# Kernel tuning notes

Hardware: AMD Instinct MI355X
Metric: run time of the kernel (lower is better)

Reference implementation:

```python
import jax, jax.numpy as jnp
import numpy as np

D_H = 128
N_RBF = 16
R_MIN = 0.0
R_MAX = float(np.sqrt(2.0))


def _rbf(r):
    # Gaussian RBF expansion: centers linspace(R_MIN, R_MAX, N_RBF),
    # width = center spacing, exp(-(r-mu)^2 / (2*width^2))
    centers = jnp.linspace(R_MIN, R_MAX, N_RBF, dtype=r.dtype)
    width = (R_MAX - R_MIN) / (N_RBF - 1)
    gamma = 1.0 / (2.0 * width * width)
    return jnp.exp(-gamma * (r[:, None] - centers[None, :]) ** 2)


def setup_inputs() -> dict:
    key = jax.random.key(0)
    ks = jax.random.split(key, 16)
    N, E = 50000, 800000
    h = jax.random.normal(ks[0], (N, D_H), dtype=jnp.float32)
    x = jax.random.uniform(ks[1], (N, 2), dtype=jnp.float32)
    edge_index = jax.random.randint(ks[2], (2, E), 0, N, dtype=jnp.int64)
    edge_weight = jax.random.uniform(ks[3], (E,), dtype=jnp.float32)

    def lin(k, fan_in, fan_out):
        s = 1.0 / np.sqrt(fan_in)
        kw, kb = jax.random.split(k)
        W = jax.random.uniform(kw, (fan_in, fan_out), minval=-s, maxval=s, dtype=jnp.float32)
        b = jax.random.uniform(kb, (fan_out,), minval=-s, maxval=s, dtype=jnp.float32)
        return W, b

    Wm1, bm1 = lin(ks[4], 2 * D_H + N_RBF, D_H)
    Wm2, bm2 = lin(ks[5], D_H, D_H)
    Wh1, bh1 = lin(ks[6], 2 * D_H, D_H)
    Wh2, bh2 = lin(ks[7], D_H, D_H)
    ln_g = jnp.ones((D_H,), dtype=jnp.float32)
    ln_b = jnp.zeros((D_H,), dtype=jnp.float32)
    return {"h": h, "x": x, "edge_index": edge_index, "edge_weight": edge_weight,
            "Wm1": Wm1, "bm1": bm1, "Wm2": Wm2, "bm2": bm2,
            "Wh1": Wh1, "bh1": bh1, "Wh2": Wh2, "bh2": bh2,
            "ln_g": ln_g, "ln_b": ln_b}


def reference(h, x, edge_index, edge_weight, Wm1, bm1, Wm2, bm2, Wh1, bh1, Wh2, bh2, ln_g, ln_b):
    N = h.shape[0]
    src = edge_index[0]
    dst = edge_index[1]
    # per-edge geometry
    dx = x[src, :2] - x[dst, :2]                      # [E,2]
    r = jnp.sqrt(jnp.sum(dx * dx, axis=-1) + 1e-8)    # [E]
    rbf = _rbf(r)                                     # [E,n_rbf]
    # message MLP: Linear -> SiLU -> Linear
    m_in = jnp.concatenate([h[src], h[dst], rbf], axis=-1)  # [E, 2*d_h+n_rbf]
    m = jax.nn.silu(m_in @ Wm1 + bm1) @ Wm2 + bm2            # [E, d_h]
    m = m * edge_weight[:, None]
    # scatter-sum aggregate into destination nodes
    agg = jax.ops.segment_sum(m, dst, num_segments=N)        # [N, d_h]
    # node update MLP
    u_in = jnp.concatenate([h, agg], axis=-1)                # [N, 2*d_h]
    h_up = jax.nn.silu(u_in @ Wh1 + bh1) @ Wh2 + bh2         # [N, d_h]
    # residual + LayerNorm
    z = h + h_up
    mu = jnp.mean(z, axis=-1, keepdims=True)
    var = jnp.var(z, axis=-1, keepdims=True)
    return (z - mu) / jnp.sqrt(var + 1e-5) * ln_g + ln_b
```

## Files before the change

kernel.cpp:

```cpp
#include <hip/hip_runtime.h>
#include <hip/hip_bf16.h>
#include <math.h>

#define DH 128
#define NRBF 16
#define EB 128
#define NTAB 1025
#define SEGCAP 32

typedef unsigned short ushort_t;
typedef __attribute__((ext_vector_type(8))) short short8;
typedef __attribute__((ext_vector_type(4))) float floatx4;

__device__ __forceinline__ float silu_f(float v) {
    return v / (1.f + __expf(-v));
}
__device__ __forceinline__ unsigned pk_bf16(float lo, float hi) {
    __hip_bfloat162 h = __float22bfloat162_rn(make_float2(lo, hi));
    union { __hip_bfloat162 h2; unsigned u; } cv;
    cv.h2 = h;
    return cv.u;
}
__device__ __forceinline__ ushort_t f2bf1(float f) {
    unsigned u = __float_as_uint(f);
    u += 0x7FFFu + ((u >> 16) & 1u);
    return (ushort_t)(u >> 16);
}
__device__ __forceinline__ float bflo(unsigned u) { return __uint_as_float(u << 16); }
__device__ __forceinline__ float bfhi(unsigned u) { return __uint_as_float(u & 0xffff0000u); }
__device__ __forceinline__ float bf2f(ushort_t u) { return __uint_as_float(((unsigned)u) << 16); }

__device__ __forceinline__ int detect64(const int* __restrict__ ei) {
    int z = 0;
#pragma unroll
    for (int i = 0; i < 8; ++i) z |= ei[2 * i + 1];
    return (z == 0) ? 1 : 0;
}
__device__ __forceinline__ int load_dst(const int* ei, int is64, int e, int E) {
    return is64 ? ei[2 * E + 2 * e] : ei[E + e];
}
__device__ __forceinline__ int load_src(const int* ei, int is64, int e, int E) {
    return is64 ? ei[2 * e] : ei[e];
}

__global__ __launch_bounds__(256) void k_hist_prep(
    const int* __restrict__ ei, int* __restrict__ counts, int E,
    const float* __restrict__ Wm1, const float* __restrict__ Wm2,
    const float* __restrict__ Wh1, const float* __restrict__ Wh2,
    ushort_t* __restrict__ Tbf, ushort_t* __restrict__ W2f,
    ushort_t* __restrict__ W1mf, ushort_t* __restrict__ W1hf,
    ushort_t* __restrict__ W2hf, int nb_hist)
{
    const int b = blockIdx.x, tid = threadIdx.x;
    if (b < nb_hist) {
        const int e = b * 256 + tid;
        if (e < E) {
            const int is64 = detect64(ei);
            atomicAdd(&counts[load_dst(ei, is64, e, E)], 1);
        }
        return;
    }
    int b2 = b - nb_hist;
    if (b2 < 257) {
        const int i = b2 * 4 + (tid >> 6);
        if (i < NTAB) {
            const float WIDTH = 0.09428090415820634f;
            const float GAMMA = 56.25f;
            const float DELTA = 1.4142135623730951f / 1024.0f;
            const float r = (float)i * DELTA;
            const int c0 = (tid & 63) * 2;
            float a0 = 0.f, a1 = 0.f;
#pragma unroll
            for (int q = 0; q < NRBF; ++q) {
                const float dr = r - (float)q * WIDTH;
                const float w = __expf(-GAMMA * dr * dr);
                a0 = fmaf(w, Wm1[(256 + q) * DH + c0], a0);
                a1 = fmaf(w, Wm1[(256 + q) * DH + c0 + 1], a1);
            }
            *(unsigned*)(Tbf + (size_t)i * DH + c0) = pk_bf16(a0, a1);
        }
        return;
    }
    b2 -= 257;
    if (b2 < 8) {
        const int u = b2 * 256 + tid;
        const int col = u & 127, kclg = u >> 7;
        const int lg = kclg & 3, kc = kclg >> 2;
        unsigned o[4];
#pragma unroll
        for (int j = 0; j < 2; ++j) {
            o[j]     = pk_bf16(Wm2[(kc * 32 + 4 * lg + 2 * j) * DH + col],
                               Wm2[(kc * 32 + 4 * lg + 2 * j + 1) * DH + col]);
            o[2 + j] = pk_bf16(Wm2[(kc * 32 + 16 + 4 * lg + 2 * j) * DH + col],
                               Wm2[(kc * 32 + 16 + 4 * lg + 2 * j + 1) * DH + col]);
        }
        *(uint4*)(W2f + 8 * u) = make_uint4(o[0], o[1], o[2], o[3]);
        return;
    }
    b2 -= 8;
    if (b2 < 16) {
        const int u = b2 * 256 + tid;
        const int c = u & 255, kclg = u >> 8;
        const int lg = kclg & 3, kc = kclg >> 2;
        const int base = (c < 128) ? 0 : 128;
        const int cc = c & 127;
        unsigned o[4];
#pragma unroll
        for (int j = 0; j < 2; ++j) {
            o[j]     = pk_bf16(Wm1[(base + kc * 32 + 4 * lg + 2 * j) * DH + cc],
                               Wm1[(base + kc * 32 + 4 * lg + 2 * j + 1) * DH + cc]);
            o[2 + j] = pk_bf16(Wm1[(base + kc * 32 + 16 + 4 * lg + 2 * j) * DH + cc],
                               Wm1[(base + kc * 32 + 16 + 4 * lg + 2 * j + 1) * DH + cc]);
        }
        *(uint4*)(W1mf + 8 * u) = make_uint4(o[0], o[1], o[2], o[3]);
        return;
    }
    b2 -= 16;
    if (b2 < 16) {
        const int u = b2 * 256 + tid;
        const int col = u & 127, kclg = u >> 7;
        const int lg = kclg & 3, kc = kclg >> 2;
        unsigned o[4];
#pragma unroll
        for (int j = 0; j < 2; ++j) {
            o[j]     = pk_bf16(Wh1[(kc * 32 + 4 * lg + 2 * j) * DH + col],
                               Wh1[(kc * 32 + 4 * lg + 2 * j + 1) * DH + col]);
            o[2 + j] = pk_bf16(Wh1[(kc * 32 + 16 + 4 * lg + 2 * j) * DH + col],
                               Wh1[(kc * 32 + 16 + 4 * lg + 2 * j + 1) * DH + col]);
        }
        *(uint4*)(W1hf + 8 * u) = make_uint4(o[0], o[1], o[2], o[3]);
        return;
    }
    b2 -= 16;
    {
        const int u = b2 * 256 + tid;
        const int col = u & 127, kclg = u >> 7;
        const int lg = kclg & 3, kc = kclg >> 2;
        unsigned o[4];
#pragma unroll
        for (int j = 0; j < 2; ++j) {
            o[j]     = pk_bf16(Wh2[(kc * 32 + 4 * lg + 2 * j) * DH + col],
                               Wh2[(kc * 32 + 4 * lg + 2 * j + 1) * DH + col]);
            o[2 + j] = pk_bf16(Wh2[(kc * 32 + 16 + 4 * lg + 2 * j) * DH + col],
                               Wh2[(kc * 32 + 16 + 4 * lg + 2 * j + 1) * DH + col]);
        }
        *(uint4*)(W2hf + 8 * u) = make_uint4(o[0], o[1], o[2], o[3]);
    }
}

__global__ __launch_bounds__(1024) void k_scan(const int* __restrict__ counts,
                                               int* __restrict__ cursor, int N) {
    __shared__ int wsum[16];
    __shared__ int sCarry;
    const int tid = threadIdx.x, lane = tid & 63, wid = tid >> 6;
    if (tid == 0) sCarry = 0;
    __syncthreads();
    for (int c0 = 0; c0 < N; c0 += 4096) {
        const int idx = c0 + tid * 4;
        int4 v = make_int4(0, 0, 0, 0);
        if (idx < N) v = *(const int4*)(counts + idx);
        const int t01 = v.x + v.y;
        const int t012 = t01 + v.z;
        const int tot = t012 + v.w;
        int incl = tot;
#pragma unroll
        for (int d = 1; d < 64; d <<= 1) {
            int t = __shfl_up(incl, d, 64);
            if (lane >= d) incl += t;
        }
        if (lane == 63) wsum[wid] = incl;
        __syncthreads();
        if (wid == 0) {
            int s = (lane < 16) ? wsum[lane] : 0;
#pragma unroll
            for (int d = 1; d < 16; d <<= 1) {
                int t = __shfl_up(s, d, 64);
                if (lane >= d) s += t;
            }
            if (lane < 16) wsum[lane] = s;
        }
        __syncthreads();
        const int ex = sCarry + (wid > 0 ? wsum[wid - 1] : 0) + incl - tot;
        if (idx + 3 < N) {
            *(int4*)(cursor + idx) = make_int4(ex, ex + v.x, ex + t01, ex + t012);
        } else if (idx < N) {
            cursor[idx] = ex;
            if (idx + 1 < N) cursor[idx + 1] = ex + v.x;
            if (idx + 2 < N) cursor[idx + 2] = ex + t01;
        }
        __syncthreads();
        if (tid == 0) sCarry += wsum[15];
        __syncthreads();
    }
}

__global__ __launch_bounds__(256) void k_scatter_pre(
    const int* __restrict__ ei, const float* __restrict__ ew, const float* __restrict__ x,
    int* __restrict__ cursor, uint2* __restrict__ spk, int* __restrict__ dstS,
    int E, int pack,
    const float* __restrict__ h, const float* __restrict__ bm1,
    const ushort_t* __restrict__ W1mf,
    ushort_t* __restrict__ Abf, ushort_t* __restrict__ Bbf, int N, int nb_scat)
{
    const int tid = threadIdx.x;

    if ((int)blockIdx.x < nb_scat) {
        const int e = blockIdx.x * 256 + tid;
        if (e < E) {
            const int is64 = detect64(ei);
            const int s = load_src(ei, is64, e, E);
            const int d = load_dst(ei, is64, e, E);
            const int pos = atomicAdd(&cursor[d], 1);
            unsigned x0 = (unsigned)s;
            if (pack) {
                const float2 xs = *(const float2*)(x + 2 * s);
                const float2 xd = *(const float2*)(x + 2 * d);
                const float dxv = xs.x - xd.x, dyv = xs.y - xd.y;
                const float r = sqrtf(dxv * dxv + dyv * dyv + 1e-8f);
                int ti = (int)(r * 724.0773439350246f + 0.5f);
                ti = min(ti, NTAB - 1);
                x0 |= ((unsigned)ti << 16);
            }
            spk[pos] = make_uint2(x0, __float_as_uint(ew[e]));
            dstS[pos] = d;
        }
        return;
    }

    __shared__ __align__(16) ushort_t sIn[64 * DH];
    const int nblk = ((int)blockIdx.x - nb_scat) * 64;

    {
        const int row = tid >> 2, q = tid & 3;
        const int gn = nblk + row;
        const float4* ps = (const float4*)(h + (size_t)gn * DH + 32 * q);
        uint4* rowp = (uint4*)(sIn + row * DH);
        const int swz = row & 7;
#pragma unroll
        for (int i = 0; i < 4; ++i) {
            uint4 o = make_uint4(0, 0, 0, 0);
            if (gn < N) {
                const float4 g0 = ps[2 * i], g1 = ps[2 * i + 1];
                o.x = pk_bf16(g0.x, g0.y); o.y = pk_bf16(g0.z, g0.w);
                o.z = pk_bf16(g1.x, g1.y); o.w = pk_bf16(g1.z, g1.w);
            }
            rowp[(4 * q + i) ^ swz] = o;
        }
    }
    __syncthreads();

    const int lane = tid & 63, wv = tid >> 6;
    const int lr = lane & 15, lg = lane >> 4;
    const int m0l = wv * 16;

    union FragU { unsigned u[4]; short8 s8; };
    floatx4 acc[16];
#pragma unroll
    for (int ni = 0; ni < 16; ++ni) acc[ni] = (floatx4){0.f, 0.f, 0.f, 0.f};

#pragma unroll
    for (int kc = 0; kc < 4; ++kc) {
        const int b1 = 64 * kc + 8 * lg;
        const int b2 = b1 + 32;
        const int row = m0l + lr;
        const char* rbase = (const char*)(sIn + row * DH);
        const int swz = (row & 7) << 4;
        FragU af;
        const uint2 lo = *(const uint2*)(rbase + ((b1 & ~15) ^ swz) + (b1 & 15));
        const uint2 hi = *(const uint2*)(rbase + ((b2 & ~15) ^ swz) + (b2 & 15));
        af.u[0] = lo.x; af.u[1] = lo.y; af.u[2] = hi.x; af.u[3] = hi.y;
        const ushort_t* wbase = W1mf + ((size_t)(kc * 4 + lg) * 256 + lr) * 8;
        __builtin_amdgcn_s_setprio(1);
#pragma unroll
        for (int ni = 0; ni < 16; ++ni) {
            const short8 bf = *(const short8*)(wbase + ni * 128);
            acc[ni] = __builtin_amdgcn_mfma_f32_16x16x32_bf16(af.s8, bf, acc[ni], 0, 0, 0);
        }
        __builtin_amdgcn_s_setprio(0);
    }

    float bm1v[8];
#pragma unroll
    for (int ni = 0; ni < 8; ++ni) bm1v[ni] = bm1[ni * 16 + lr];
#pragma unroll
    for (int r = 0; r < 4; ++r) {
        const int gn = nblk + m0l + 4 * lg + r;
        if (gn < N) {
#pragma unroll
            for (int ni = 0; ni < 8; ++ni)
                Abf[(size_t)gn * DH + ni * 16 + lr] = f2bf1(acc[ni][r] + bm1v[ni]);
#pragma unroll
            for (int ni = 8; ni < 16; ++ni)
                Bbf[(size_t)gn * DH + (ni - 8) * 16 + lr] = f2bf1(acc[ni][r]);
        }
    }
}

__global__ __launch_bounds__(256, 4) void k_edge(
    const float* __restrict__ x, const int* __restrict__ ei, const float* __restrict__ ew,
    const uint2* __restrict__ spk, const int* __restrict__ dstS,
    const ushort_t* __restrict__ W2f, const float* __restrict__ bm2,
    const ushort_t* __restrict__ Abf, const ushort_t* __restrict__ Bbf,
    const ushort_t* __restrict__ Tbf, float* __restrict__ agg,
    int sorted, int pack, int N, int E)
{
    __shared__ __align__(16) ushort_t sHid[64 * DH];
    __shared__ __align__(16) float ldsAgg[SEGCAP][DH];
    __shared__ int   sSrc[EB];
    __shared__ int   sDst[EB];
    __shared__ int   sLid[EB];
    __shared__ int   sTi[EB];
    __shared__ float sEw[EB];
    __shared__ int   sSegStart[SEGCAP];
    __shared__ int   sNseg, sW0tot;

    const int tid = threadIdx.x;

    const int nwg = gridDim.x;
    const int xcd = blockIdx.x & 7;
    const int cidx = blockIdx.x >> 3;
    const int qch = nwg >> 3, rch = nwg & 7;
    const int bid = (xcd < rch) ? (xcd * (qch + 1) + cidx)
                                : (rch * (qch + 1) + (xcd - rch) * qch + cidx);
    const int e0 = bid * EB;

    {
        const float4 z = make_float4(0.f, 0.f, 0.f, 0.f);
        float4* za = (float4*)&ldsAgg[0][0];
#pragma unroll
        for (int i = 0; i < 4; ++i) za[tid + 256 * i] = z;
    }

    if (tid < EB) {
        const int slot = e0 + tid;
        int s = 0, d = 0, ti = 0;
        float w = 0.f;
        if (slot < E) {
            if (sorted) {
                const uint2 v = spk[slot];
                d = dstS[slot];
                w = __uint_as_float(v.y);
                if (pack) { s = (int)(v.x & 0xFFFFu); ti = (int)(v.x >> 16); }
                else {
                    s = (int)v.x;
                    const float2 xs = *(const float2*)(x + 2 * s);
                    const float2 xd = *(const float2*)(x + 2 * d);
                    const float dxv = xs.x - xd.x, dyv = xs.y - xd.y;
                    const float r = sqrtf(dxv * dxv + dyv * dyv + 1e-8f);
                    ti = min((int)(r * 724.0773439350246f + 0.5f), NTAB - 1);
                }
            } else {
                const int is64 = detect64(ei);
                s = load_src(ei, is64, slot, E);
                d = load_dst(ei, is64, slot, E);
                w = ew[slot];
                const float2 xs = *(const float2*)(x + 2 * s);
                const float2 xd = *(const float2*)(x + 2 * d);
                const float dxv = xs.x - xd.x, dyv = xs.y - xd.y;
                const float r = sqrtf(dxv * dxv + dyv * dyv + 1e-8f);
                ti = min((int)(r * 724.0773439350246f + 0.5f), NTAB - 1);
            }
        } else {
            d = sorted ? dstS[E - 1] : load_dst(ei, detect64(ei), E - 1, E);
        }
        sSrc[tid] = s; sDst[tid] = d; sEw[tid] = w; sTi[tid] = ti;
    }
    __syncthreads();

    int bflag = 0, incl = 0;
    if (tid < EB) {
        bflag = (tid > 0) && (sDst[tid] != sDst[tid - 1]);
        incl = bflag;
#pragma unroll
        for (int dd = 1; dd < 64; dd <<= 1) {
            int t = __shfl_up(incl, dd, 64);
            if ((tid & 63) >= dd) incl += t;
        }
    }
    if (tid == 63) sW0tot = incl;
    __syncthreads();
    if (tid >= 64 && tid < EB) incl += sW0tot;
    if (tid < EB) {
        sLid[tid] = incl;
        if ((bflag || tid == 0) && incl < SEGCAP) sSegStart[incl] = tid;
        if (tid == EB - 1) sNseg = incl + 1;
    }
    __syncthreads();

    const int lane = tid & 63;
    const int wv   = tid >> 6;
    const int lr   = lane & 15;
    const int lg   = lane >> 4;
    const int m0l  = (wv & 1) * 32;
    const int n0   = (wv >> 1) * 64;

    float bc4[4];
#pragma unroll
    for (int ni = 0; ni < 4; ++ni) bc4[ni] = bm2[n0 + ni * 16 + lr];

    union FragU { unsigned u[4]; short8 s8; };

    for (int half = 0; half < 2; ++half) {
        const int eh = half * 64;

        {
            const int el = tid >> 2;
            const int q  = tid & 3;
            const int le = eh + el;
            const int s  = sSrc[le];
            const int ti = sTi[le];
            const uint4* pA = (const uint4*)(Abf + (size_t)s * DH + 32 * q);
            const uint4* pB = (const uint4*)(Bbf + (size_t)sDst[le] * DH + 32 * q);
            const uint4* pT = (const uint4*)(Tbf + (size_t)ti * DH + 32 * q);
            uint4* rowp = (uint4*)(sHid + el * DH);
            const int swz = el & 7;
#pragma unroll
            for (int i = 0; i < 4; ++i) {
                const uint4 a = pA[i];
                const uint4 b = pB[i];
                const uint4 t = pT[i];
                const float v0 = bflo(a.x) + bflo(b.x) + bflo(t.x);
                const float v1 = bfhi(a.x) + bfhi(b.x) + bfhi(t.x);
                const float v2 = bflo(a.y) + bflo(b.y) + bflo(t.y);
                const float v3 = bfhi(a.y) + bfhi(b.y) + bfhi(t.y);
                const float v4 = bflo(a.z) + bflo(b.z) + bflo(t.z);
                const float v5 = bfhi(a.z) + bfhi(b.z) + bfhi(t.z);
                const float v6 = bflo(a.w) + bflo(b.w) + bflo(t.w);
                const float v7 = bfhi(a.w) + bfhi(b.w) + bfhi(t.w);
                uint4 pk;
                pk.x = pk_bf16(silu_f(v0), silu_f(v1));
                pk.y = pk_bf16(silu_f(v2), silu_f(v3));
                pk.z = pk_bf16(silu_f(v4), silu_f(v5));
                pk.w = pk_bf16(silu_f(v6), silu_f(v7));
                rowp[(4 * q + i) ^ swz] = pk;
            }
        }
        __syncthreads();

        floatx4 acc[2][4];
#pragma unroll
        for (int mi = 0; mi < 2; ++mi)
#pragma unroll
            for (int ni = 0; ni < 4; ++ni) acc[mi][ni] = (floatx4){0.f, 0.f, 0.f, 0.f};

#pragma unroll
        for (int kc = 0; kc < 4; ++kc) {
            const int b1 = 64 * kc + 8 * lg;
            const int b2 = b1 + 32;
            FragU af[2];
#pragma unroll
            for (int mi = 0; mi < 2; ++mi) {
                const int le2 = m0l + mi * 16 + lr;
                const char* rbase = (const char*)(sHid + le2 * DH);
                const int swz = (le2 & 7) << 4;
                const uint2 lo = *(const uint2*)(rbase + ((b1 & ~15) ^ swz) + (b1 & 15));
                const uint2 hi = *(const uint2*)(rbase + ((b2 & ~15) ^ swz) + (b2 & 15));
                af[mi].u[0] = lo.x; af[mi].u[1] = lo.y;
                af[mi].u[2] = hi.x; af[mi].u[3] = hi.y;
            }
            const ushort_t* wbase = W2f + ((size_t)(kc * 4 + lg) * 128 + n0 + lr) * 8;
            __builtin_amdgcn_s_setprio(1);
#pragma unroll
            for (int ni = 0; ni < 4; ++ni) {
                const short8 bf = *(const short8*)(wbase + ni * 128);
                acc[0][ni] = __builtin_amdgcn_mfma_f32_16x16x32_bf16(af[0].s8, bf, acc[0][ni], 0, 0, 0);
                acc[1][ni] = __builtin_amdgcn_mfma_f32_16x16x32_bf16(af[1].s8, bf, acc[1][ni], 0, 0, 0);
            }
            __builtin_amdgcn_s_setprio(0);
        }

        int   lid4[2][4];
        float ew4[2][4];
        int   hs[2];
#pragma unroll
        for (int mi = 0; mi < 2; ++mi) {
            const int sb = eh + m0l + mi * 16 + 4 * lg;
            hs[mi] = sb;
#pragma unroll
            for (int r = 0; r < 4; ++r) { lid4[mi][r] = sLid[sb + r]; ew4[mi][r] = sEw[sb + r]; }
        }
#pragma unroll
        for (int ni = 0; ni < 4; ++ni) {
            const int col = n0 + ni * 16 + lr;
            const float bc = bc4[ni];
#pragma unroll
            for (int mi = 0; mi < 2; ++mi) {
                int cur = lid4[mi][0], curSlot = hs[mi];
                float av = (acc[mi][ni][0] + bc) * ew4[mi][0];
#pragma unroll
                for (int r = 1; r < 4; ++r) {
                    const int l2 = lid4[mi][r];
                    const float v = (acc[mi][ni][r] + bc) * ew4[mi][r];
                    if (l2 == cur) av += v;
                    else {
                        if (cur < SEGCAP) atomicAdd(&ldsAgg[cur][col], av);
                        else atomicAdd(agg + (size_t)sDst[curSlot] * DH + col, av);
                        cur = l2; curSlot = hs[mi] + r; av = v;
                    }
                }
                if (cur < SEGCAP) atomicAdd(&ldsAgg[cur][col], av);
                else atomicAdd(agg + (size_t)sDst[curSlot] * DH + col, av);
            }
        }
        __syncthreads();
    }

    const int ns = sNseg;
    const int gmax = (ns < SEGCAP) ? ns : SEGCAP;
    for (int idx = tid; idx < (gmax << 7); idx += 256) {
        const int g = idx >> 7, col = idx & 127;
        const float v = ldsAgg[g][col];
        const int dst = sDst[sSegStart[g]];
        float* p = agg + (size_t)dst * DH + col;
        if (sorted && g > 0 && g < ns - 1) *p = v;
        else atomicAdd(p, v);
    }
}

__global__ __launch_bounds__(256) void k_node(
    const float* __restrict__ h, const float* __restrict__ agg,
    const ushort_t* __restrict__ W1hf, const float* __restrict__ bh1,
    const ushort_t* __restrict__ W2hf, const float* __restrict__ bh2,
    const float* __restrict__ ln_g, const float* __restrict__ ln_b,
    float* __restrict__ out, int N)
{
    __shared__ __align__(16) ushort_t sIn[64 * 256];
    __shared__ __align__(16) ushort_t sHid[64 * DH];
    const int tid = threadIdx.x;
    const int nblk = blockIdx.x * 64;

    {
        const int row = tid >> 2, q = tid & 3;
        const int gn = nblk + row;
        const float4* ps = (q < 2) ? (const float4*)(h + (size_t)gn * DH + 64 * q)
                                   : (const float4*)(agg + (size_t)gn * DH + 64 * (q - 2));
        uint4* rowp = (uint4*)(sIn + row * 256);
        const int swz = row & 7;
#pragma unroll
        for (int i = 0; i < 8; ++i) {
            uint4 o = make_uint4(0, 0, 0, 0);
            if (gn < N) {
                const float4 g0 = ps[2 * i], g1 = ps[2 * i + 1];
                o.x = pk_bf16(g0.x, g0.y); o.y = pk_bf16(g0.z, g0.w);
                o.z = pk_bf16(g1.x, g1.y); o.w = pk_bf16(g1.z, g1.w);
            }
            rowp[(8 * q + i) ^ swz] = o;
        }
    }
    __syncthreads();

    const int lane = tid & 63, wv = tid >> 6;
    const int lr = lane & 15, lg = lane >> 4;
    const int m0l = wv * 16;

    union FragU { unsigned u[4]; short8 s8; };

    floatx4 acc[8];
#pragma unroll
    for (int ni = 0; ni < 8; ++ni) acc[ni] = (floatx4){0.f, 0.f, 0.f, 0.f};

#pragma unroll
    for (int kc = 0; kc < 8; ++kc) {
        const int b1 = 64 * kc + 8 * lg;
        const int b2 = b1 + 32;
        const int row = m0l + lr;
        const char* rbase = (const char*)(sIn + row * 256);
        const int swz = (row & 7) << 4;
        FragU af;
        const uint2 lo = *(const uint2*)(rbase + ((b1 & ~15) ^ swz) + (b1 & 15));
        const uint2 hi = *(const uint2*)(rbase + ((b2 & ~15) ^ swz) + (b2 & 15));
        af.u[0] = lo.x; af.u[1] = lo.y; af.u[2] = hi.x; af.u[3] = hi.y;
        const ushort_t* wbase = W1hf + ((size_t)(kc * 4 + lg) * 128 + lr) * 8;
        __builtin_amdgcn_s_setprio(1);
#pragma unroll
        for (int ni = 0; ni < 8; ++ni) {
            const short8 bf = *(const short8*)(wbase + ni * 128);
            acc[ni] = __builtin_amdgcn_mfma_f32_16x16x32_bf16(af.s8, bf, acc[ni], 0, 0, 0);
        }
        __builtin_amdgcn_s_setprio(0);
    }

    {
        float bh1v[8];
#pragma unroll
        for (int ni = 0; ni < 8; ++ni) bh1v[ni] = bh1[ni * 16 + lr];
#pragma unroll
        for (int r = 0; r < 4; ++r) {
            const int row = m0l + 4 * lg + r;
            const int swz = row & 7;
            ushort_t* rp = sHid + row * DH;
#pragma unroll
            for (int ni = 0; ni < 8; ++ni) {
                const int col = ni * 16 + lr;
                rp[(((col >> 3) ^ swz) << 3) + (col & 7)] =
                    f2bf1(silu_f(acc[ni][r] + bh1v[ni]));
            }
        }
    }

    floatx4 acc2[8];
#pragma unroll
    for (int ni = 0; ni < 8; ++ni) acc2[ni] = (floatx4){0.f, 0.f, 0.f, 0.f};

#pragma unroll
    for (int kc = 0; kc < 4; ++kc) {
        const int b1 = 64 * kc + 8 * lg;
        const int b2 = b1 + 32;
        const int row = m0l + lr;
        const char* rbase = (const char*)(sHid + row * DH);
        const int swz = (row & 7) << 4;
        FragU af;
        const uint2 lo = *(const uint2*)(rbase + ((b1 & ~15) ^ swz) + (b1 & 15));
        const uint2 hi = *(const uint2*)(rbase + ((b2 & ~15) ^ swz) + (b2 & 15));
        af.u[0] = lo.x; af.u[1] = lo.y; af.u[2] = hi.x; af.u[3] = hi.y;
        const ushort_t* wbase = W2hf + ((size_t)(kc * 4 + lg) * 128 + lr) * 8;
        __builtin_amdgcn_s_setprio(1);
#pragma unroll
        for (int ni = 0; ni < 8; ++ni) {
            const short8 bf = *(const short8*)(wbase + ni * 128);
            acc2[ni] = __builtin_amdgcn_mfma_f32_16x16x32_bf16(af.s8, bf, acc2[ni], 0, 0, 0);
        }
        __builtin_amdgcn_s_setprio(0);
    }

    float gv[8], bv[8], b2v[8];
#pragma unroll
    for (int ni = 0; ni < 8; ++ni) {
        const int col = ni * 16 + lr;
        gv[ni] = ln_g[col]; bv[ni] = ln_b[col]; b2v[ni] = bh2[col];
    }
#pragma unroll
    for (int r = 0; r < 4; ++r) {
        const int row = m0l + 4 * lg + r;
        const int gn = nblk + row;
        const int swz = row & 7;
        float z[8];
        float s1 = 0.f, s2 = 0.f;
#pragma unroll
        for (int ni = 0; ni < 8; ++ni) {
            const int col = ni * 16 + lr;
            const float hv = bf2f(sIn[row * 256 + (((col >> 3) ^ swz) << 3) + (col & 7)]);
            z[ni] = acc2[ni][r] + b2v[ni] + hv;
            s1 += z[ni]; s2 += z[ni] * z[ni];
        }
#pragma unroll
        for (int m = 1; m < 16; m <<= 1) {
            s1 += __shfl_xor(s1, m, 64);
            s2 += __shfl_xor(s2, m, 64);
        }
        const float mean = s1 * (1.f / 128.f);
        const float var = s2 * (1.f / 128.f) - mean * mean;
        const float rstd = rsqrtf(var + 1e-5f);
        if (gn < N) {
#pragma unroll
            for (int ni = 0; ni < 8; ++ni) {
                const int col = ni * 16 + lr;
                out[(size_t)gn * DH + col] = (z[ni] - mean) * rstd * gv[ni] + bv[ni];
            }
        }
    }
}

extern "C" void kernel_launch(void* const* d_in, const int* in_sizes, int n_in,
                              void* d_out, int out_size, void* d_ws, size_t ws_size,
                              hipStream_t stream)
{
    (void)n_in; (void)out_size;
    const float* h   = (const float*)d_in[0];
    const float* x   = (const float*)d_in[1];
    const int*   ei  = (const int*)d_in[2];
    const float* ew  = (const float*)d_in[3];
    const float* Wm1 = (const float*)d_in[4];
    const float* bm1 = (const float*)d_in[5];
    const float* Wm2 = (const float*)d_in[6];
    const float* bm2 = (const float*)d_in[7];
    const float* Wh1 = (const float*)d_in[8];
    const float* bh1 = (const float*)d_in[9];
    const float* Wh2 = (const float*)d_in[10];
    const float* bh2 = (const float*)d_in[11];
    const float* lng = (const float*)d_in[12];
    const float* lnb = (const float*)d_in[13];
    float* out = (float*)d_out;

    const int N = in_sizes[0] / DH;
    const int E = in_sizes[3];

    float*    agg  = (float*)d_ws;
    ushort_t* Abf  = (ushort_t*)(agg + (size_t)N * DH);
    ushort_t* Bbf  = Abf + (size_t)N * DH;
    ushort_t* W2f  = Bbf + (size_t)N * DH;
    ushort_t* Tbf  = W2f + 16384;
    ushort_t* W1mf = Tbf + (size_t)NTAB * DH;
    ushort_t* W1hf = W1mf + 32768;
    ushort_t* W2hf = W1hf + 32768;
    int*   counts  = (int*)(W2hf + 16384);
    int*   cursor  = counts + N;
    uint2* spk     = (uint2*)(cursor + N);
    int*   dstS    = (int*)(spk + E);

    const size_t mand = (size_t)N * DH * 4 + (size_t)N * DH * 4
                      + ((size_t)16384 + (size_t)NTAB * DH + 32768 + 32768 + 16384) * 2;
    const size_t need = mand + (size_t)(2 * N) * 4 + (size_t)E * 12 + 64;
    const int use_sort = (ws_size >= need) ? 1 : 0;
    const int pack = use_sort && (N <= 65535);

    const int nb_hist = use_sort ? (E + 255) / 256 : 0;
    const int nb_prep = 257 + 8 + 16 + 16 + 8;
    const int nb_scat = nb_hist;
    const int nb_pre  = (N + 63) / 64;

    hipMemsetAsync(agg, 0, (size_t)N * DH * sizeof(float), stream);
    if (use_sort)
        hipMemsetAsync(counts, 0, (size_t)N * sizeof(int), stream);
    k_hist_prep<<<nb_hist + nb_prep, 256, 0, stream>>>(ei, counts, E, Wm1, Wm2, Wh1, Wh2,
                                                       Tbf, W2f, W1mf, W1hf, W2hf, nb_hist);
    if (use_sort)
        k_scan<<<1, 1024, 0, stream>>>(counts, cursor, N);
    k_scatter_pre<<<nb_scat + nb_pre, 256, 0, stream>>>(ei, ew, x, cursor, spk, dstS, E, pack,
                                                        h, bm1, W1mf, Abf, Bbf, N, nb_scat);
    k_edge<<<(E + EB - 1) / EB, 256, 0, stream>>>(x, ei, ew, spk, dstS,
                                                  W2f, bm2, Abf, Bbf, Tbf, agg,
                                                  use_sort, pack, N, E);
    k_node<<<(N + 63) / 64, 256, 0, stream>>>(h, agg, W1hf, bh1, W2hf, bh2, lng, lnb, out, N);
}
```

Baseline: 436.8 us.

## Restructure edge kernel into per-wave 16-edge tiles with early prefetched gathers

```diff
diff --git a/kernel.cpp b/kernel.cpp
--- a/kernel.cpp
+++ b/kernel.cpp
@@ -304,7 +304,7 @@
     const ushort_t* __restrict__ Tbf, float* __restrict__ agg,
     int sorted, int pack, int N, int E)
 {
-    __shared__ __align__(16) ushort_t sHid[64 * DH];
+    __shared__ __align__(16) ushort_t sHid[4][16 * DH];
     __shared__ __align__(16) float ldsAgg[SEGCAP][DH];
     __shared__ int   sSrc[EB];
     __shared__ int   sDst[EB];
@@ -314,7 +314,14 @@
     __shared__ int   sSegStart[SEGCAP];
     __shared__ int   sNseg, sW0tot;
 
-    const int tid = threadIdx.x;
+    const int tid  = threadIdx.x;
+    const int lane = tid & 63;
+    const int wv   = tid >> 6;
+    const int lr   = lane & 15;
+    const int lg   = lane >> 4;
+    const int e4   = lane >> 2;
+    const int q    = lane & 3;
+    const int wbase = wv * 32;
 
     const int nwg = gridDim.x;
     const int xcd = blockIdx.x & 7;
@@ -323,6 +330,29 @@
     const int bid = (xcd < rch) ? (xcd * (qch + 1) + cidx)
                                 : (rch * (qch + 1) + (xcd - rch) * qch + cidx);
     const int e0 = bid * EB;
+
+    const int fast = sorted && pack;
+
+    uint4 a0[4], b0[4], t0v[4], a1[4], b1[4], t1v[4];
+    int d1g = 0, t1g = 0;
+    if (fast) {
+        const int sl0 = min(e0 + wbase + e4, E - 1);
+        const int sl1 = min(e0 + wbase + 16 + e4, E - 1);
+        const uint2 v0 = spk[sl0], v1 = spk[sl1];
+        const int s0g = (int)(v0.x & 0xFFFFu), t0g = (int)(v0.x >> 16);
+        const int s1g = (int)(v1.x & 0xFFFFu);
+        t1g = (int)(v1.x >> 16);
+        const int d0g = dstS[sl0];
+        d1g = dstS[sl1];
+        const uint4* pA0 = (const uint4*)(Abf + (size_t)s0g * DH + 32 * q);
+        const uint4* pB0 = (const uint4*)(Bbf + (size_t)d0g * DH + 32 * q);
+        const uint4* pT0 = (const uint4*)(Tbf + (size_t)t0g * DH + 32 * q);
+        const uint4* pA1 = (const uint4*)(Abf + (size_t)s1g * DH + 32 * q);
+#pragma unroll
+        for (int i = 0; i < 4; ++i) {
+            a0[i] = pA0[i]; b0[i] = pB0[i]; t0v[i] = pT0[i]; a1[i] = pA1[i];
+        }
+    }
 
     {
         const float4 z = make_float4(0.f, 0.f, 0.f, 0.f);
@@ -387,123 +417,122 @@
     }
     __syncthreads();
 
-    const int lane = tid & 63;
-    const int wv   = tid >> 6;
-    const int lr   = lane & 15;
-    const int lg   = lane >> 4;
-    const int m0l  = (wv & 1) * 32;
-    const int n0   = (wv >> 1) * 64;
-
-    float bc4[4];
-#pragma unroll
-    for (int ni = 0; ni < 4; ++ni) bc4[ni] = bm2[n0 + ni * 16 + lr];
+    if (!fast) {
+        const int le0 = wbase + e4;
+        const int s0g = sSrc[le0], d0g = sDst[le0], t0g = sTi[le0];
+        const uint4* pA0 = (const uint4*)(Abf + (size_t)s0g * DH + 32 * q);
+        const uint4* pB0 = (const uint4*)(Bbf + (size_t)d0g * DH + 32 * q);
+        const uint4* pT0 = (const uint4*)(Tbf + (size_t)t0g * DH + 32 * q);
+#pragma unroll
+        for (int i = 0; i < 4; ++i) { a0[i] = pA0[i]; b0[i] = pB0[i]; t0v[i] = pT0[i]; }
+        const int le1 = wbase + 16 + e4;
+        const int s1g = sSrc[le1];
+        d1g = sDst[le1]; t1g = sTi[le1];
+        const uint4* pA1 = (const uint4*)(Abf + (size_t)s1g * DH + 32 * q);
+#pragma unroll
+        for (int i = 0; i < 4; ++i) a1[i] = pA1[i];
+    }
+
+    float bc8[8];
+#pragma unroll
+    for (int ni = 0; ni < 8; ++ni) bc8[ni] = bm2[ni * 16 + lr];
 
     union FragU { unsigned u[4]; short8 s8; };
-
-    for (int half = 0; half < 2; ++half) {
-        const int eh = half * 64;
-
-        {
-            const int el = tid >> 2;
-            const int q  = tid & 3;
-            const int le = eh + el;
-            const int s  = sSrc[le];
-            const int ti = sTi[le];
-            const uint4* pA = (const uint4*)(Abf + (size_t)s * DH + 32 * q);
-            const uint4* pB = (const uint4*)(Bbf + (size_t)sDst[le] * DH + 32 * q);
-            const uint4* pT = (const uint4*)(Tbf + (size_t)ti * DH + 32 * q);
-            uint4* rowp = (uint4*)(sHid + el * DH);
-            const int swz = el & 7;
-#pragma unroll
-            for (int i = 0; i < 4; ++i) {
-                const uint4 a = pA[i];
-                const uint4 b = pB[i];
-                const uint4 t = pT[i];
-                const float v0 = bflo(a.x) + bflo(b.x) + bflo(t.x);
-                const float v1 = bfhi(a.x) + bfhi(b.x) + bfhi(t.x);
-                const float v2 = bflo(a.y) + bflo(b.y) + bflo(t.y);
-                const float v3 = bfhi(a.y) + bfhi(b.y) + bfhi(t.y);
-                const float v4 = bflo(a.z) + bflo(b.z) + bflo(t.z);
-                const float v5 = bfhi(a.z) + bfhi(b.z) + bfhi(t.z);
-                const float v6 = bflo(a.w) + bflo(b.w) + bflo(t.w);
-                const float v7 = bfhi(a.w) + bfhi(b.w) + bfhi(t.w);
-                uint4 pk;
-                pk.x = pk_bf16(silu_f(v0), silu_f(v1));
-                pk.y = pk_bf16(silu_f(v2), silu_f(v3));
-                pk.z = pk_bf16(silu_f(v4), silu_f(v5));
-                pk.w = pk_bf16(silu_f(v6), silu_f(v7));
-                rowp[(4 * q + i) ^ swz] = pk;
-            }
-        }
-        __syncthreads();
-
-        floatx4 acc[2][4];
-#pragma unroll
-        for (int mi = 0; mi < 2; ++mi)
-#pragma unroll
-            for (int ni = 0; ni < 4; ++ni) acc[mi][ni] = (floatx4){0.f, 0.f, 0.f, 0.f};
-
-#pragma unroll
-        for (int kc = 0; kc < 4; ++kc) {
-            const int b1 = 64 * kc + 8 * lg;
-            const int b2 = b1 + 32;
-            FragU af[2];
-#pragma unroll
-            for (int mi = 0; mi < 2; ++mi) {
-                const int le2 = m0l + mi * 16 + lr;
-                const char* rbase = (const char*)(sHid + le2 * DH);
-                const int swz = (le2 & 7) << 4;
-                const uint2 lo = *(const uint2*)(rbase + ((b1 & ~15) ^ swz) + (b1 & 15));
-                const uint2 hi = *(const uint2*)(rbase + ((b2 & ~15) ^ swz) + (b2 & 15));
-                af[mi].u[0] = lo.x; af[mi].u[1] = lo.y;
-                af[mi].u[2] = hi.x; af[mi].u[3] = hi.y;
-            }
-            const ushort_t* wbase = W2f + ((size_t)(kc * 4 + lg) * 128 + n0 + lr) * 8;
-            __builtin_amdgcn_s_setprio(1);
-#pragma unroll
-            for (int ni = 0; ni < 4; ++ni) {
-                const short8 bf = *(const short8*)(wbase + ni * 128);
-                acc[0][ni] = __builtin_amdgcn_mfma_f32_16x16x32_bf16(af[0].s8, bf, acc[0][ni], 0, 0, 0);
-                acc[1][ni] = __builtin_amdgcn_mfma_f32_16x16x32_bf16(af[1].s8, bf, acc[1][ni], 0, 0, 0);
-            }
-            __builtin_amdgcn_s_setprio(0);
-        }
-
-        int   lid4[2][4];
-        float ew4[2][4];
-        int   hs[2];
-#pragma unroll
-        for (int mi = 0; mi < 2; ++mi) {
-            const int sb = eh + m0l + mi * 16 + 4 * lg;
-            hs[mi] = sb;
-#pragma unroll
-            for (int r = 0; r < 4; ++r) { lid4[mi][r] = sLid[sb + r]; ew4[mi][r] = sEw[sb + r]; }
-        }
-#pragma unroll
-        for (int ni = 0; ni < 4; ++ni) {
-            const int col = n0 + ni * 16 + lr;
-            const float bc = bc4[ni];
-#pragma unroll
-            for (int mi = 0; mi < 2; ++mi) {
-                int cur = lid4[mi][0], curSlot = hs[mi];
-                float av = (acc[mi][ni][0] + bc) * ew4[mi][0];
-#pragma unroll
-                for (int r = 1; r < 4; ++r) {
-                    const int l2 = lid4[mi][r];
-                    const float v = (acc[mi][ni][r] + bc) * ew4[mi][r];
-                    if (l2 == cur) av += v;
-                    else {
-                        if (cur < SEGCAP) atomicAdd(&ldsAgg[cur][col], av);
-                        else atomicAdd(agg + (size_t)sDst[curSlot] * DH + col, av);
-                        cur = l2; curSlot = hs[mi] + r; av = v;
-                    }
-                }
-                if (cur < SEGCAP) atomicAdd(&ldsAgg[cur][col], av);
-                else atomicAdd(agg + (size_t)sDst[curSlot] * DH + col, av);
-            }
-        }
-        __syncthreads();
-    }
+    ushort_t* slice = &sHid[wv][0];
+    floatx4 acc[8];
+
+#define BUILD_HID(aA, bB, tT)                                                   \
+    {                                                                           \
+        uint4* rowp = (uint4*)(slice + e4 * DH);                                \
+        const int swzw = e4 & 7;                                                \
+        _Pragma("unroll")                                                       \
+        for (int i = 0; i < 4; ++i) {                                           \
+            const uint4 a = aA[i]; const uint4 b = bB[i]; const uint4 t = tT[i];\
+            const float v0 = bflo(a.x) + bflo(b.x) + bflo(t.x);                 \
+            const float v1 = bfhi(a.x) + bfhi(b.x) + bfhi(t.x);                 \
+            const float v2 = bflo(a.y) + bflo(b.y) + bflo(t.y);                 \
+            const float v3 = bfhi(a.y) + bfhi(b.y) + bfhi(t.y);                 \
+            const float v4 = bflo(a.z) + bflo(b.z) + bflo(t.z);                 \
+            const float v5 = bfhi(a.z) + bfhi(b.z) + bfhi(t.z);                 \
+            const float v6 = bflo(a.w) + bflo(b.w) + bflo(t.w);                 \
+            const float v7 = bfhi(a.w) + bfhi(b.w) + bfhi(t.w);                 \
+            uint4 pk;                                                           \
+            pk.x = pk_bf16(silu_f(v0), silu_f(v1));                             \
+            pk.y = pk_bf16(silu_f(v2), silu_f(v3));                             \
+            pk.z = pk_bf16(silu_f(v4), silu_f(v5));                             \
+            pk.w = pk_bf16(silu_f(v6), silu_f(v7));                             \
+            rowp[(4 * q + i) ^ swzw] = pk;                                      \
+        }                                                                       \
+    }
+
+#define MFMA_ST()                                                               \
+    {                                                                           \
+        _Pragma("unroll")                                                       \
+        for (int ni = 0; ni < 8; ++ni) acc[ni] = (floatx4){0.f, 0.f, 0.f, 0.f}; \
+        _Pragma("unroll")                                                       \
+        for (int kc = 0; kc < 4; ++kc) {                                        \
+            const int bo1 = 64 * kc + 8 * lg;                                   \
+            const int bo2 = bo1 + 32;                                           \
+            const char* rbase = (const char*)(slice + lr * DH);                 \
+            const int swzf = (lr & 7) << 4;                                     \
+            FragU af;                                                           \
+            const uint2 lo = *(const uint2*)(rbase + ((bo1 & ~15) ^ swzf) + (bo1 & 15)); \
+            const uint2 hi = *(const uint2*)(rbase + ((bo2 & ~15) ^ swzf) + (bo2 & 15)); \
+            af.u[0] = lo.x; af.u[1] = lo.y; af.u[2] = hi.x; af.u[3] = hi.y;     \
+            const ushort_t* wb2 = W2f + ((size_t)(kc * 4 + lg) * 128 + lr) * 8; \
+            __builtin_amdgcn_s_setprio(1);                                      \
+            _Pragma("unroll")                                                   \
+            for (int ni = 0; ni < 8; ++ni) {                                    \
+                const short8 bf = *(const short8*)(wb2 + ni * 128);             \
+                acc[ni] = __builtin_amdgcn_mfma_f32_16x16x32_bf16(af.s8, bf, acc[ni], 0, 0, 0); \
+            }                                                                   \
+            __builtin_amdgcn_s_setprio(0);                                      \
+        }                                                                       \
+    }
+
+#define PHASE3(ST)                                                              \
+    {                                                                           \
+        const int sb = wbase + (ST) * 16 + 4 * lg;                              \
+        int lid4[4]; float ew4[4];                                              \
+        _Pragma("unroll")                                                       \
+        for (int r = 0; r < 4; ++r) { lid4[r] = sLid[sb + r]; ew4[r] = sEw[sb + r]; } \
+        _Pragma("unroll")                                                       \
+        for (int ni = 0; ni < 8; ++ni) {                                        \
+            const int col = ni * 16 + lr;                                       \
+            const float bc = bc8[ni];                                           \
+            int cur = lid4[0], curSlot = sb;                                    \
+            float av = (acc[ni][0] + bc) * ew4[0];                              \
+            _Pragma("unroll")                                                   \
+            for (int r = 1; r < 4; ++r) {                                       \
+                const int l2 = lid4[r];                                         \
+                const float v = (acc[ni][r] + bc) * ew4[r];                     \
+                if (l2 == cur) av += v;                                         \
+                else {                                                          \
+                    if (cur < SEGCAP) atomicAdd(&ldsAgg[cur][col], av);         \
+                    else atomicAdd(agg + (size_t)sDst[curSlot] * DH + col, av); \
+                    cur = l2; curSlot = sb + r; av = v;                         \
+                }                                                               \
+            }                                                                   \
+            if (cur < SEGCAP) atomicAdd(&ldsAgg[cur][col], av);                 \
+            else atomicAdd(agg + (size_t)sDst[curSlot] * DH + col, av);         \
+        }                                                                       \
+    }
+
+    BUILD_HID(a0, b0, t0v);
+    MFMA_ST();
+    {
+        const uint4* pB1 = (const uint4*)(Bbf + (size_t)d1g * DH + 32 * q);
+        const uint4* pT1 = (const uint4*)(Tbf + (size_t)t1g * DH + 32 * q);
+#pragma unroll
+        for (int i = 0; i < 4; ++i) { b1[i] = pB1[i]; t1v[i] = pT1[i]; }
+    }
+    PHASE3(0);
+
+    BUILD_HID(a1, b1, t1v);
+    MFMA_ST();
+    PHASE3(1);
+
+    __syncthreads();
 
     const int ns = sNseg;
     const int gmax = (ns < SEGCAP) ? ns : SEGCAP;
@@ -515,6 +544,9 @@
         if (sorted && g > 0 && g < ns - 1) *p = v;
         else atomicAdd(p, v);
     }
+#undef BUILD_HID
+#undef MFMA_ST
+#undef PHASE3
 }
 
 __global__ __launch_bounds__(256) void k_node(
```

New measurement: 415.5 us. 4.9% less time.

## Restructure edge kernel into per-wave 16-edge tiles with register-resident W2

Applied to the files above, without the earlier changes.

```diff
diff --git a/kernel.cpp b/kernel.cpp
--- a/kernel.cpp
+++ b/kernel.cpp
@@ -4,7 +4,7 @@
 
 #define DH 128
 #define NRBF 16
-#define EB 128
+#define EB 256
 #define NTAB 1025
 #define SEGCAP 32
 
@@ -296,7 +296,7 @@
     }
 }
 
-__global__ __launch_bounds__(256, 4) void k_edge(
+__global__ __launch_bounds__(256, 2) void k_edge(
     const float* __restrict__ x, const int* __restrict__ ei, const float* __restrict__ ew,
     const uint2* __restrict__ spk, const int* __restrict__ dstS,
     const ushort_t* __restrict__ W2f, const float* __restrict__ bm2,
@@ -304,7 +304,7 @@
     const ushort_t* __restrict__ Tbf, float* __restrict__ agg,
     int sorted, int pack, int N, int E)
 {
-    __shared__ __align__(16) ushort_t sHid[64 * DH];
+    __shared__ __align__(16) ushort_t sHid[4][16 * DH];
     __shared__ __align__(16) float ldsAgg[SEGCAP][DH];
     __shared__ int   sSrc[EB];
     __shared__ int   sDst[EB];
@@ -312,9 +312,17 @@
     __shared__ int   sTi[EB];
     __shared__ float sEw[EB];
     __shared__ int   sSegStart[SEGCAP];
-    __shared__ int   sNseg, sW0tot;
-
-    const int tid = threadIdx.x;
+    __shared__ int   sNseg;
+    __shared__ int   sWtot[4];
+
+    const int tid  = threadIdx.x;
+    const int lane = tid & 63;
+    const int wv   = tid >> 6;
+    const int lr   = lane & 15;
+    const int lg   = lane >> 4;
+    const int e4   = lane >> 2;
+    const int q    = lane & 3;
+    const int wbase = wv * 64;
 
     const int nwg = gridDim.x;
     const int xcd = blockIdx.x & 7;
@@ -324,6 +332,18 @@
                                 : (rch * (qch + 1) + (xcd - rch) * qch + cidx);
     const int e0 = bid * EB;
 
+    const int fast = sorted && pack;
+
+    union FragU { unsigned u[4]; short8 s8; };
+
+    FragU bfr[4][8];
+#pragma unroll
+    for (int kc = 0; kc < 4; ++kc)
+#pragma unroll
+        for (int ni = 0; ni < 8; ++ni)
+            *(uint4*)bfr[kc][ni].u =
+                *(const uint4*)(W2f + ((size_t)(kc * 4 + lg) * 128 + ni * 16 + lr) * 8);
+
     {
         const float4 z = make_float4(0.f, 0.f, 0.f, 0.f);
         float4* za = (float4*)&ldsAgg[0][0];
@@ -331,7 +351,7 @@
         for (int i = 0; i < 4; ++i) za[tid + 256 * i] = z;
     }
 
-    if (tid < EB) {
+    {
         const int slot = e0 + tid;
         int s = 0, d = 0, ti = 0;
         float w = 0.f;
@@ -367,58 +387,55 @@
     }
     __syncthreads();
 
-    int bflag = 0, incl = 0;
-    if (tid < EB) {
-        bflag = (tid > 0) && (sDst[tid] != sDst[tid - 1]);
-        incl = bflag;
+    {
+        const int bflag = (tid > 0) && (sDst[tid] != sDst[tid - 1]);
+        int incl = bflag;
 #pragma unroll
         for (int dd = 1; dd < 64; dd <<= 1) {
             int t = __shfl_up(incl, dd, 64);
-            if ((tid & 63) >= dd) incl += t;
-        }
-    }
-    if (tid == 63) sW0tot = incl;
-    __syncthreads();
-    if (tid >= 64 && tid < EB) incl += sW0tot;
-    if (tid < EB) {
+            if (lane >= dd) incl += t;
+        }
+        if (lane == 63) sWtot[wv] = incl;
+        __syncthreads();
+        int off = 0;
+#pragma unroll
+        for (int wq = 0; wq < 3; ++wq)
+            if (wq < wv) off += sWtot[wq];
+        incl += off;
         sLid[tid] = incl;
         if ((bflag || tid == 0) && incl < SEGCAP) sSegStart[incl] = tid;
         if (tid == EB - 1) sNseg = incl + 1;
     }
     __syncthreads();
 
-    const int lane = tid & 63;
-    const int wv   = tid >> 6;
-    const int lr   = lane & 15;
-    const int lg   = lane >> 4;
-    const int m0l  = (wv & 1) * 32;
-    const int n0   = (wv >> 1) * 64;
-
-    float bc4[4];
-#pragma unroll
-    for (int ni = 0; ni < 4; ++ni) bc4[ni] = bm2[n0 + ni * 16 + lr];
-
-    union FragU { unsigned u[4]; short8 s8; };
-
-    for (int half = 0; half < 2; ++half) {
-        const int eh = half * 64;
+    float bc8[8];
+#pragma unroll
+    for (int ni = 0; ni < 8; ++ni) bc8[ni] = bm2[ni * 16 + lr];
+
+    ushort_t* slice = &sHid[wv][0];
+    floatx4 acc[8];
+
+#pragma unroll
+    for (int st = 0; st < 4; ++st) {
+        const int sb = wbase + st * 16;
+
+        const int le = sb + e4;
+        const int s  = sSrc[le];
+        const int d  = sDst[le];
+        const int ti = sTi[le];
+        const uint4* pA = (const uint4*)(Abf + (size_t)s * DH + 32 * q);
+        const uint4* pB = (const uint4*)(Bbf + (size_t)d * DH + 32 * q);
+        const uint4* pT = (const uint4*)(Tbf + (size_t)ti * DH + 32 * q);
+        uint4 av[4], bv[4], tv[4];
+#pragma unroll
+        for (int i = 0; i < 4; ++i) { av[i] = pA[i]; bv[i] = pB[i]; tv[i] = pT[i]; }
 
         {
-            const int el = tid >> 2;
-            const int q  = tid & 3;
-            const int le = eh + el;
-            const int s  = sSrc[le];
-            const int ti = sTi[le];
-            const uint4* pA = (const uint4*)(Abf + (size_t)s * DH + 32 * q);
-            const uint4* pB = (const uint4*)(Bbf + (size_t)sDst[le] * DH + 32 * q);
-            const uint4* pT = (const uint4*)(Tbf + (size_t)ti * DH + 32 * q);
-            uint4* rowp = (uint4*)(sHid + el * DH);
-            const int swz = el & 7;
+            uint4* rowp = (uint4*)(slice + e4 * DH);
+            const int swzw = e4 & 7;
 #pragma unroll
             for (int i = 0; i < 4; ++i) {
-                const uint4 a = pA[i];
-                const uint4 b = pB[i];
-                const uint4 t = pT[i];
+                const uint4 a = av[i]; const uint4 b = bv[i]; const uint4 t = tv[i];
                 const float v0 = bflo(a.x) + bflo(b.x) + bflo(t.x);
                 const float v1 = bfhi(a.x) + bfhi(b.x) + bfhi(t.x);
                 const float v2 = bflo(a.y) + bflo(b.y) + bflo(t.y);
@@ -432,78 +449,58 @@
                 pk.y = pk_bf16(silu_f(v2), silu_f(v3));
                 pk.z = pk_bf16(silu_f(v4), silu_f(v5));
                 pk.w = pk_bf16(silu_f(v6), silu_f(v7));
-                rowp[(4 * q + i) ^ swz] = pk;
-            }
-        }
-        __syncthreads();
-
-        floatx4 acc[2][4];
-#pragma unroll
-        for (int mi = 0; mi < 2; ++mi)
-#pragma unroll
-            for (int ni = 0; ni < 4; ++ni) acc[mi][ni] = (floatx4){0.f, 0.f, 0.f, 0.f};
-
+                rowp[(4 * q + i) ^ swzw] = pk;
+            }
+        }
+
+#pragma unroll
+        for (int ni = 0; ni < 8; ++ni) acc[ni] = (floatx4){0.f, 0.f, 0.f, 0.f};
 #pragma unroll
         for (int kc = 0; kc < 4; ++kc) {
-            const int b1 = 64 * kc + 8 * lg;
-            const int b2 = b1 + 32;
-            FragU af[2];
-#pragma unroll
-            for (int mi = 0; mi < 2; ++mi) {
-                const int le2 = m0l + mi * 16 + lr;
-                const char* rbase = (const char*)(sHid + le2 * DH);
-                const int swz = (le2 & 7) << 4;
-                const uint2 lo = *(const uint2*)(rbase + ((b1 & ~15) ^ swz) + (b1 & 15));
-                const uint2 hi = *(const uint2*)(rbase + ((b2 & ~15) ^ swz) + (b2 & 15));
-                af[mi].u[0] = lo.x; af[mi].u[1] = lo.y;
-                af[mi].u[2] = hi.x; af[mi].u[3] = hi.y;
-            }
-            const ushort_t* wbase = W2f + ((size_t)(kc * 4 + lg) * 128 + n0 + lr) * 8;
+            const int bo1 = 64 * kc + 8 * lg;
+            const int bo2 = bo1 + 32;
+            const char* rbase = (const char*)(slice + lr * DH);
+            const int swzf = (lr & 7) << 4;
+            FragU af;
+            const uint2 lo = *(const uint2*)(rbase + ((bo1 & ~15) ^ swzf) + (bo1 & 15));
+            const uint2 hi = *(const uint2*)(rbase + ((bo2 & ~15) ^ swzf) + (bo2 & 15));
+            af.u[0] = lo.x; af.u[1] = lo.y; af.u[2] = hi.x; af.u[3] = hi.y;
             __builtin_amdgcn_s_setprio(1);
 #pragma unroll
-            for (int ni = 0; ni < 4; ++ni) {
-                const short8 bf = *(const short8*)(wbase + ni * 128);
-                acc[0][ni] = __builtin_amdgcn_mfma_f32_16x16x32_bf16(af[0].s8, bf, acc[0][ni], 0, 0, 0);
-                acc[1][ni] = __builtin_amdgcn_mfma_f32_16x16x32_bf16(af[1].s8, bf, acc[1][ni], 0, 0, 0);
-            }
+            for (int ni = 0; ni < 8; ++ni)
+                acc[ni] = __builtin_amdgcn_mfma_f32_16x16x32_bf16(af.s8, bfr[kc][ni].s8, acc[ni], 0, 0, 0);
             __builtin_amdgcn_s_setprio(0);
         }
 
-        int   lid4[2][4];
-        float ew4[2][4];
-        int   hs[2];
-#pragma unroll
-        for (int mi = 0; mi < 2; ++mi) {
-            const int sb = eh + m0l + mi * 16 + 4 * lg;
-            hs[mi] = sb;
-#pragma unroll
-            for (int r = 0; r < 4; ++r) { lid4[mi][r] = sLid[sb + r]; ew4[mi][r] = sEw[sb + r]; }
-        }
-#pragma unroll
-        for (int ni = 0; ni < 4; ++ni) {
-            const int col = n0 + ni * 16 + lr;
-            const float bc = bc4[ni];
-#pragma unroll
-            for (int mi = 0; mi < 2; ++mi) {
-                int cur = lid4[mi][0], curSlot = hs[mi];
-                float av = (acc[mi][ni][0] + bc) * ew4[mi][0];
+        {
+            const int sbg = sb + 4 * lg;
+            int lid4[4]; float ew4[4];
+#pragma unroll
+            for (int r = 0; r < 4; ++r) { lid4[r] = sLid[sbg + r]; ew4[r] = sEw[sbg + r]; }
+#pragma unroll
+            for (int ni = 0; ni < 8; ++ni) {
+                const int col = ni * 16 + lr;
+                const float bc = bc8[ni];
+                int cur = lid4[0], curSlot = sbg;
+                float avv = (acc[ni][0] + bc) * ew4[0];
 #pragma unroll
                 for (int r = 1; r < 4; ++r) {
-                    const int l2 = lid4[mi][r];
-                    const float v = (acc[mi][ni][r] + bc) * ew4[mi][r];
-                    if (l2 == cur) av += v;
+                    const int l2 = lid4[r];
+                    const float v = (acc[ni][r] + bc) * ew4[r];
+                    if (l2 == cur) avv += v;
                     else {
-                        if (cur < SEGCAP) atomicAdd(&ldsAgg[cur][col], av);
-                        else atomicAdd(agg + (size_t)sDst[curSlot] * DH + col, av);
-                        cur = l2; curSlot = hs[mi] + r; av = v;
+                        if (cur < SEGCAP) atomicAdd(&ldsAgg[cur][col], avv);
+                        else atomicAdd(agg + (size_t)sDst[curSlot] * DH + col, avv);
+                        cur = l2; curSlot = sbg + r; avv = v;
                     }
                 }
-                if (cur < SEGCAP) atomicAdd(&ldsAgg[cur][col], av);
-                else atomicAdd(agg + (size_t)sDst[curSlot] * DH + col, av);
-            }
-        }
-        __syncthreads();
-    }
+                if (cur < SEGCAP) atomicAdd(&ldsAgg[cur][col], avv);
+                else atomicAdd(agg + (size_t)sDst[curSlot] * DH + col, avv);
+            }
+        }
+    }
+
+    __syncthreads();
 
     const int ns = sNseg;
     const int gmax = (ns < SEGCAP) ? ns : SEGCAP;
```

New measurement: 396.9 us (median of 2 runs). -9.1%, faster.
